# Kernel optimization log

Measured on AMD Instinct MI355X. Metric: run time of the kernel, lower is better.

The kernel has to match this reference:

```python
import jax, jax.numpy as jnp
import numpy as np

B, N, D, H = 4, 2048, 1024, 16
HD = D // H


def setup_inputs() -> dict:
    key = jax.random.key(0)
    ks = jax.random.split(key, 9)
    s = 1.0 / np.sqrt(D)
    return {
        "x": jax.random.normal(ks[0], (B, N, D), jnp.float32),
        "Wq": jax.random.normal(ks[1], (D, D), jnp.float32) * s,
        "bq": jnp.zeros((D,), jnp.float32),
        "Wk": jax.random.normal(ks[2], (D, D), jnp.float32) * s,
        "bk": jnp.zeros((D,), jnp.float32),
        "Wv": jax.random.normal(ks[3], (D, D), jnp.float32) * s,
        "bv": jnp.zeros((D,), jnp.float32),
        "Wo": jax.random.normal(ks[4], (D, D), jnp.float32) * s,
        "bo": jnp.zeros((D,), jnp.float32),
    }


def reference(x, Wq, bq, Wk, bk, Wv, bv, Wo, bo):
    Bx, Nx, Dx = x.shape
    q = x @ Wq + bq  # [B,N,D]
    k = x @ Wk + bk
    v = x @ Wv + bv
    # split heads -> [B,H,N,hd]
    q = q.reshape(Bx, Nx, H, HD).transpose(0, 2, 1, 3)
    k = k.reshape(Bx, Nx, H, HD).transpose(0, 2, 1, 3)
    v = v.reshape(Bx, Nx, H, HD).transpose(0, 2, 1, 3)
    q = q / jnp.sqrt(jnp.asarray(HD, q.dtype))
    scores = jnp.einsum("bhqd,bhkd->bhqk", q, k)
    # causal mask: additive -1e9 strictly above diagonal (matches torch.triu diag=1)
    mask = jnp.triu(jnp.full((Nx, Nx), -1e9, dtype=scores.dtype), k=1)
    probs = jax.nn.softmax(scores + mask, axis=-1)
    out = jnp.einsum("bhqk,bhkd->bhqd", probs, v)  # [B,H,N,hd]
    out = out.transpose(0, 2, 1, 3).reshape(Bx, Nx, Dx)  # concat heads
    return out @ Wo + bo
```

## Files before the change

### kernel.cpp

```cpp
#include <hip/hip_runtime.h>
#include <hip/hip_bf16.h>


#define BB 4
#define NN 2048
#define DD 1024
#define HH 16
#define HD 64
#define MM (BB * NN)

typedef __bf16 bf16;
typedef __bf16 bf16x4 __attribute__((ext_vector_type(4)));
typedef __bf16 bf16x8 __attribute__((ext_vector_type(8)));
typedef float f32x4 __attribute__((ext_vector_type(4)));

__device__ __forceinline__ void async_copy16(bf16* lds, const bf16* g) {
    __builtin_amdgcn_global_load_lds(
        (const __attribute__((address_space(1))) void*)g,
        (__attribute__((address_space(3))) void*)lds, 16, 0, 0);
}

__global__ void prep(const float* __restrict__ x,
                     const float* __restrict__ W0, const float* __restrict__ W1,
                     const float* __restrict__ W2, const float* __restrict__ W3,
                     bf16* __restrict__ xb, bf16* __restrict__ Wt) {
    __shared__ float tile[32][33];
    if (blockIdx.z == 0) {
        int i = (blockIdx.x * 256 + threadIdx.x) * 8;
        float4 a = *(const float4*)&x[i];
        float4 b = *(const float4*)&x[i + 4];
        bf16x8 o;
        o[0] = (bf16)a.x; o[1] = (bf16)a.y; o[2] = (bf16)a.z; o[3] = (bf16)a.w;
        o[4] = (bf16)b.x; o[5] = (bf16)b.y; o[6] = (bf16)b.z; o[7] = (bf16)b.w;
        *(bf16x8*)&xb[i] = o;
    } else {
        int wz = blockIdx.x >> 10;
        int by = (blockIdx.x >> 5) & 31;
        int bx = blockIdx.x & 31;
        const float* W = (wz == 0) ? W0 : (wz == 1) ? W1 : (wz == 2) ? W2 : W3;
        bf16* out = Wt + (size_t)wz * DD * DD;
        int tx = threadIdx.x & 31, ty = threadIdx.x >> 5;
        int x0 = bx * 32, y0 = by * 32;
#pragma unroll
        for (int i = 0; i < 32; i += 8)
            tile[ty + i][tx] = W[(size_t)(y0 + ty + i) * DD + x0 + tx];
        __syncthreads();
#pragma unroll
        for (int i = 0; i < 32; i += 8)
            out[(size_t)(x0 + ty + i) * DD + y0 + tx] = (bf16)tile[tx][ty + i];
    }
}

__global__ __launch_bounds__(512, 4) void gemm_qkv(
    const bf16* __restrict__ A, const bf16* __restrict__ Wt,
    const float* __restrict__ b0, const float* __restrict__ b1,
    const float* __restrict__ b2, bf16* __restrict__ out0,
    bf16* __restrict__ out1, bf16* __restrict__ out2) {
    const int K = DD;
    __shared__ __align__(16) bf16 smem[128 * 136];
    bf16* As = smem;
    bf16* Bs = smem + 256 * 32;
    bf16* Cs = smem;

    int m0 = blockIdx.x * 256;
    int n0 = blockIdx.y * 128;
    int z = blockIdx.z;
    const bf16* Wz = Wt + (size_t)z * DD * DD;
    const float* bias = (z == 0) ? b0 : ((z == 1) ? b1 : b2);
    bf16* out = (z == 0) ? out0 : ((z == 1) ? out1 : out2);
    float scale = (z == 0) ? 0.125f * 1.44269504f : 1.0f;

    int tid = threadIdx.x;
    int w = tid >> 6, lane = tid & 63;
    int wm = w >> 1, wn = w & 1;
    int quad = lane >> 4, l16 = lane & 15;

    f32x4 acc[4][4];
#pragma unroll
    for (int i = 0; i < 4; i++)
#pragma unroll
        for (int j = 0; j < 4; j++) acc[i][j] = (f32x4){0.f, 0.f, 0.f, 0.f};

    for (int k0 = 0; k0 < K; k0 += 32) {
        __syncthreads();
#pragma unroll
        for (int j = 0; j < 2; j++) {
            int c = j * 512 + tid;
            int row = c >> 2, kk = (c & 3) * 8;
            async_copy16(&As[c * 8], &A[(size_t)(m0 + row) * K + k0 + kk]);
        }
        {
            int row = tid >> 2, kk = (tid & 3) * 8;
            async_copy16(&Bs[tid * 8], &Wz[(size_t)(n0 + row) * K + k0 + kk]);
        }
        __syncthreads();

        bf16x8 af[4], bfm[4];
#pragma unroll
        for (int i = 0; i < 4; i++) {
            af[i] = *(const bf16x8*)&As[(wm * 64 + i * 16 + l16) * 32 + quad * 8];
            bfm[i] = *(const bf16x8*)&Bs[(wn * 64 + i * 16 + l16) * 32 + quad * 8];
        }
#pragma unroll
        for (int i = 0; i < 4; i++)
#pragma unroll
            for (int j = 0; j < 4; j++)
                acc[i][j] = __builtin_amdgcn_mfma_f32_16x16x32_bf16(
                    af[i], bfm[j], acc[i][j], 0, 0, 0);
    }

    int bidx = m0 >> 11;
    int tok0 = m0 & (NN - 1);
    int hh0 = n0 >> 6;
    __syncthreads();

#pragma unroll
    for (int pp = 0; pp < 2; pp++) {
        if (pp) __syncthreads();
        if ((wm >> 1) == pp) {
#pragma unroll
            for (int j = 0; j < 4; j++) {
                int nl = wn * 64 + j * 16 + l16;
                float bv = bias[n0 + nl];
#pragma unroll
                for (int i = 0; i < 4; i++) {
#pragma unroll
                    for (int r = 0; r < 4; r++) {
                        int mloc = (wm & 1) * 64 + i * 16 + quad * 4 + r;
                        bf16 v = (bf16)((acc[i][j][r] + bv) * scale);
                        if (z == 2) Cs[nl * 136 + mloc] = v;
                        else        Cs[mloc * 136 + nl] = v;
                    }
                }
            }
        }
        __syncthreads();

        if (z != 2) {
#pragma unroll
            for (int hf = 0; hf < 2; hf++) {
                bf16* base = out +
                    ((size_t)(bidx * HH + hh0 + hf) * NN + tok0 + pp * 128) * HD;
#pragma unroll
                for (int k = 0; k < 2; k++) {
                    int f = k * 4096 + tid * 8;
                    *(bf16x8*)&base[f] =
                        *(const bf16x8*)&Cs[(f >> 6) * 136 + hf * 64 + (f & 63)];
                }
            }
        } else {
#pragma unroll
            for (int k = 0; k < 4; k++) {
                int idx = k * 4096 + tid * 8;
                int nl = idx >> 7;
                int p0 = idx & 127;
                int hf = nl >> 6, hd = nl & 63;
                int base32 = p0 & ~31;
                int qq = (p0 & 31) >> 3;
                const bf16* crow = &Cs[nl * 136];
                bf16x4 lo = *(const bf16x4*)&crow[base32 + qq * 4];
                bf16x4 hi = *(const bf16x4*)&crow[base32 + qq * 4 + 16];
                bf16x8 v = __builtin_shufflevector(lo, hi, 0, 1, 2, 3, 4, 5, 6, 7);
                bf16* dst = out +
                    ((size_t)(bidx * HH + hh0 + hf) * HD + hd) * NN +
                    tok0 + pp * 128 + p0;
                *(bf16x8*)dst = v;
            }
        }
    }
}

__global__ __launch_bounds__(256) void gemm_out(
    const bf16* __restrict__ A, const bf16* __restrict__ Wt,
    const float* __restrict__ bias, float* __restrict__ out) {
    const int K = DD;
    __shared__ __align__(16) bf16 smem[128 * 64];
    bf16* As = smem;
    bf16* Bs = smem + 128 * 32;

    int m0 = blockIdx.x * 128;
    int n0 = blockIdx.y * 128;

    int tid = threadIdx.x;
    int w = tid >> 6, lane = tid & 63;
    int wm = w >> 1, wn = w & 1;
    int quad = lane >> 4, l16 = lane & 15;

    f32x4 acc[4][4];
#pragma unroll
    for (int i = 0; i < 4; i++)
#pragma unroll
        for (int j = 0; j < 4; j++) acc[i][j] = (f32x4){0.f, 0.f, 0.f, 0.f};

    for (int k0 = 0; k0 < K; k0 += 32) {
        __syncthreads();
#pragma unroll
        for (int j = 0; j < 2; j++) {
            int c = j * 256 + w * 64 + lane;
            int row = c >> 2, kk = (c & 3) * 8;
            async_copy16(&As[c * 8], &A[(size_t)(m0 + row) * K + k0 + kk]);
            async_copy16(&Bs[c * 8], &Wt[(size_t)(n0 + row) * K + k0 + kk]);
        }
        __syncthreads();

        bf16x8 af[4], bfm[4];
#pragma unroll
        for (int i = 0; i < 4; i++) {
            af[i] = *(const bf16x8*)&As[(wm * 64 + i * 16 + l16) * 32 + quad * 8];
            bfm[i] = *(const bf16x8*)&Bs[(wn * 64 + i * 16 + l16) * 32 + quad * 8];
        }
#pragma unroll
        for (int i = 0; i < 4; i++)
#pragma unroll
            for (int j = 0; j < 4; j++)
                acc[i][j] = __builtin_amdgcn_mfma_f32_16x16x32_bf16(
                    af[i], bfm[j], acc[i][j], 0, 0, 0);
    }

#pragma unroll
    for (int j = 0; j < 4; j++) {
        int n = n0 + wn * 64 + j * 16 + l16;
        float bv = bias[n];
#pragma unroll
        for (int i = 0; i < 4; i++) {
            int mrow = m0 + wm * 64 + i * 16 + quad * 4;
#pragma unroll
            for (int r = 0; r < 4; r++)
                out[(size_t)(mrow + r) * DD + n] = acc[i][j][r] + bv;
        }
    }
}

__global__ __launch_bounds__(256, 4) void flash_attn(
    const bf16* __restrict__ Q, const bf16* __restrict__ Kg,
    const bf16* __restrict__ Vt_g, bf16* __restrict__ Oc) {
    __shared__ __align__(16) bf16 Ks[2][64 * 72];
    __shared__ __align__(16) bf16 Vs[2][64 * 72];

    int bh = blockIdx.x;
    int b = bh >> 4, h = bh & 15;
    int tid = threadIdx.x;
    int w = tid >> 6, lane = tid & 63;
    int quad = lane >> 4, l16 = lane & 15;

    const bf16* Qb = Q + (size_t)bh * NN * HD;
    const bf16* Kb = Kg + (size_t)bh * NN * HD;
    const bf16* Vtb = Vt_g + (size_t)bh * HD * NN;

    bf16x8 ones8;
#pragma unroll
    for (int i = 0; i < 8; i++) ones8[i] = (bf16)1.0f;

    int kr[2], kc[2];
#pragma unroll
    for (int j = 0; j < 2; j++) {
        int c = j * 256 + tid;
        kr[j] = c >> 3; kc[j] = (c & 7) * 8;
    }

    for (int phase = 0; phase < 2; phase++) {
        int qj = (phase == 0) ? blockIdx.y : (31 - blockIdx.y);
        int q0 = qj * 64;
        int qrow = q0 + w * 16 + l16;

        bf16x8 qf[2];
#pragma unroll
        for (int ks = 0; ks < 2; ks++)
            qf[ks] = *(const bf16x8*)&Qb[(size_t)qrow * HD + ks * 32 + quad * 8];

        f32x4 l_sum = (f32x4){0.f, 0.f, 0.f, 0.f};
        f32x4 o_acc[4];
#pragma unroll
        for (int di = 0; di < 4; di++) o_acc[di] = (f32x4){0.f, 0.f, 0.f, 0.f};

        bf16x8 kreg[2], vreg[2];
#pragma unroll
        for (int j = 0; j < 2; j++) {
            kreg[j] = *(const bf16x8*)&Kb[(size_t)kr[j] * HD + kc[j]];
            vreg[j] = *(const bf16x8*)&Vtb[(size_t)kr[j] * NN + kc[j]];
        }
#pragma unroll
        for (int j = 0; j < 2; j++) {
            *(bf16x8*)&Ks[0][kr[j] * 72 + kc[j]] = kreg[j];
            *(bf16x8*)&Vs[0][kr[j] * 72 + kc[j]] = vreg[j];
        }
        __syncthreads();

        for (int t = 0; t <= qj; t++) {
            int cur = t & 1;
            if (t < qj) {
                int kvn = (t + 1) * 64;
#pragma unroll
                for (int j = 0; j < 2; j++) {
                    kreg[j] = *(const bf16x8*)&Kb[(size_t)(kvn + kr[j]) * HD + kc[j]];
                    vreg[j] = *(const bf16x8*)&Vtb[(size_t)kr[j] * NN + kvn + kc[j]];
                }
            }

            const bf16* Kcur = Ks[cur];
            const bf16* Vcur = Vs[cur];
            int kv0 = t * 64;
            bool diag = (t == qj);
#pragma unroll
            for (int mi = 0; mi < 2; mi++) {
                int ba = 2 * mi, bb = 2 * mi + 1;
                bf16x8 ka0 = *(const bf16x8*)&Kcur[(ba * 16 + l16) * 72 + quad * 8];
                bf16x8 ka1 = *(const bf16x8*)&Kcur[(ba * 16 + l16) * 72 + 32 + quad * 8];
                bf16x8 kb0 = *(const bf16x8*)&Kcur[(bb * 16 + l16) * 72 + quad * 8];
                bf16x8 kb1 = *(const bf16x8*)&Kcur[(bb * 16 + l16) * 72 + 32 + quad * 8];
                f32x4 sa = (f32x4){0.f, 0.f, 0.f, 0.f};
                f32x4 sb = (f32x4){0.f, 0.f, 0.f, 0.f};
                sa = __builtin_amdgcn_mfma_f32_16x16x32_bf16(ka0, qf[0], sa, 0, 0, 0);
                sa = __builtin_amdgcn_mfma_f32_16x16x32_bf16(ka1, qf[1], sa, 0, 0, 0);
                sb = __builtin_amdgcn_mfma_f32_16x16x32_bf16(kb0, qf[0], sb, 0, 0, 0);
                sb = __builtin_amdgcn_mfma_f32_16x16x32_bf16(kb1, qf[1], sb, 0, 0, 0);
                bf16x4 pa4, pb4;
                if (diag) {
                    int kva = kv0 + ba * 16 + quad * 4;
                    int kvb = kv0 + bb * 16 + quad * 4;
#pragma unroll
                    for (int r = 0; r < 4; r++) {
                        pa4[r] = (bf16)((kva + r > qrow) ? 0.f : exp2f(sa[r]));
                        pb4[r] = (bf16)((kvb + r > qrow) ? 0.f : exp2f(sb[r]));
                    }
                } else {
#pragma unroll
                    for (int r = 0; r < 4; r++) {
                        pa4[r] = (bf16)exp2f(sa[r]);
                        pb4[r] = (bf16)exp2f(sb[r]);
                    }
                }
                bf16x8 pfrag = __builtin_shufflevector(pa4, pb4, 0, 1, 2, 3, 4, 5, 6, 7);
                l_sum = __builtin_amdgcn_mfma_f32_16x16x32_bf16(pfrag, ones8, l_sum, 0, 0, 0);
#pragma unroll
                for (int di = 0; di < 4; di++) {
                    bf16x8 vfrag = *(const bf16x8*)&Vcur[(di * 16 + l16) * 72 + mi * 32 + quad * 8];
                    o_acc[di] = __builtin_amdgcn_mfma_f32_16x16x32_bf16(pfrag, vfrag, o_acc[di], 0, 0, 0);
                }
            }

            if (t < qj) {
                bf16* Kn = Ks[cur ^ 1];
                bf16* Vn = Vs[cur ^ 1];
#pragma unroll
                for (int j = 0; j < 2; j++) {
                    *(bf16x8*)&Kn[kr[j] * 72 + kc[j]] = kreg[j];
                    *(bf16x8*)&Vn[kr[j] * 72 + kc[j]] = vreg[j];
                }
            }
            __syncthreads();
        }

#pragma unroll
        for (int r = 0; r < 4; r++) {
            float inv = 1.0f / l_sum[r];
            int tok = q0 + w * 16 + quad * 4 + r;
#pragma unroll
            for (int di = 0; di < 4; di++) {
                int d = h * 64 + di * 16 + l16;
                Oc[((size_t)(b * NN + tok)) * DD + d] = (bf16)(o_acc[di][r] * inv);
            }
        }
    }
}

extern "C" void kernel_launch(void* const* d_in, const int* in_sizes, int n_in,
                              void* d_out, int out_size, void* d_ws, size_t ws_size,
                              hipStream_t stream) {
    const float* x  = (const float*)d_in[0];
    const float* Wq = (const float*)d_in[1];
    const float* bq = (const float*)d_in[2];
    const float* Wk = (const float*)d_in[3];
    const float* bk = (const float*)d_in[4];
    const float* Wv = (const float*)d_in[5];
    const float* bv = (const float*)d_in[6];
    const float* Wo = (const float*)d_in[7];
    const float* bo = (const float*)d_in[8];

    const size_t need = (size_t)(8388608ull * 5 + 4194304ull) * sizeof(bf16);
    if (ws_size < need) return;

    bf16* ws = (bf16*)d_ws;
    bf16* xb = ws;
    bf16* wt = xb + (size_t)MM * DD;
    bf16* Qw = wt + 4ull * DD * DD;
    bf16* Kw = Qw + (size_t)MM * DD;
    bf16* Vw = Kw + (size_t)MM * DD;
    bf16* Aw = Vw + (size_t)MM * DD;

    prep<<<dim3(4096, 1, 2), 256, 0, stream>>>(x, Wq, Wk, Wv, Wo, xb, wt);

    gemm_qkv<<<dim3(MM / 256, DD / 128, 3), 512, 0, stream>>>(
        xb, wt, bq, bk, bv, Qw, Kw, Vw);

    flash_attn<<<dim3(BB * HH, 16), 256, 0, stream>>>(Qw, Kw, Vw, Aw);

    gemm_out<<<dim3(MM / 128, DD / 128), 256, 0, stream>>>(
        Aw, wt + 3ull * DD * DD, bo, (float*)d_out);
}
```

Baseline: 265.0 us.

## Fuse Q/K/V projections into one block sharing the loaded A tile

The QKV GEMM no longer launches one grid slice per projection. Each 256-thread block now loads a 128-row tile of x once and multiplies it against all three weight tiles, holding three accumulator sets. This cuts global and LDS traffic for the activation matrix. In exchange the block keeps 192 accumulator floats per thread, has fewer threads and blocks (launch bounds 256,1), and runs three serialized epilogues, so occupancy and register pressure may suffer.

```diff
diff --git a/kernel.cpp b/kernel.cpp
--- a/kernel.cpp
+++ b/kernel.cpp
@@ -51,7 +51,7 @@
     }
 }
 
-__global__ __launch_bounds__(512, 4) void gemm_qkv(
+__global__ __launch_bounds__(256, 1) void gemm_qkv(
     const bf16* __restrict__ A, const bf16* __restrict__ Wt,
     const float* __restrict__ b0, const float* __restrict__ b1,
     const float* __restrict__ b2, bf16* __restrict__ out0,
@@ -59,54 +59,57 @@
     const int K = DD;
     __shared__ __align__(16) bf16 smem[128 * 136];
     bf16* As = smem;
-    bf16* Bs = smem + 256 * 32;
+    bf16* Bs = smem + 4096;
     bf16* Cs = smem;
 
-    int m0 = blockIdx.x * 256;
+    int m0 = blockIdx.x * 128;
     int n0 = blockIdx.y * 128;
-    int z = blockIdx.z;
-    const bf16* Wz = Wt + (size_t)z * DD * DD;
-    const float* bias = (z == 0) ? b0 : ((z == 1) ? b1 : b2);
-    bf16* out = (z == 0) ? out0 : ((z == 1) ? out1 : out2);
-    float scale = (z == 0) ? 0.125f * 1.44269504f : 1.0f;
 
     int tid = threadIdx.x;
     int w = tid >> 6, lane = tid & 63;
     int wm = w >> 1, wn = w & 1;
     int quad = lane >> 4, l16 = lane & 15;
 
-    f32x4 acc[4][4];
-#pragma unroll
-    for (int i = 0; i < 4; i++)
-#pragma unroll
-        for (int j = 0; j < 4; j++) acc[i][j] = (f32x4){0.f, 0.f, 0.f, 0.f};
+    f32x4 acc[3][4][4];
+#pragma unroll
+    for (int zz = 0; zz < 3; zz++)
+#pragma unroll
+        for (int i = 0; i < 4; i++)
+#pragma unroll
+            for (int j = 0; j < 4; j++)
+                acc[zz][i][j] = (f32x4){0.f, 0.f, 0.f, 0.f};
 
     for (int k0 = 0; k0 < K; k0 += 32) {
         __syncthreads();
 #pragma unroll
         for (int j = 0; j < 2; j++) {
-            int c = j * 512 + tid;
+            int c = j * 256 + w * 64 + lane;
             int row = c >> 2, kk = (c & 3) * 8;
             async_copy16(&As[c * 8], &A[(size_t)(m0 + row) * K + k0 + kk]);
-        }
-        {
-            int row = tid >> 2, kk = (tid & 3) * 8;
-            async_copy16(&Bs[tid * 8], &Wz[(size_t)(n0 + row) * K + k0 + kk]);
-        }
-        __syncthreads();
-
-        bf16x8 af[4], bfm[4];
-#pragma unroll
-        for (int i = 0; i < 4; i++) {
+#pragma unroll
+            for (int zz = 0; zz < 3; zz++)
+                async_copy16(&Bs[zz * 4096 + c * 8],
+                             &Wt[(size_t)zz * DD * DD + (size_t)(n0 + row) * K + k0 + kk]);
+        }
+        __syncthreads();
+
+        bf16x8 af[4];
+#pragma unroll
+        for (int i = 0; i < 4; i++)
             af[i] = *(const bf16x8*)&As[(wm * 64 + i * 16 + l16) * 32 + quad * 8];
-            bfm[i] = *(const bf16x8*)&Bs[(wn * 64 + i * 16 + l16) * 32 + quad * 8];
-        }
-#pragma unroll
-        for (int i = 0; i < 4; i++)
-#pragma unroll
-            for (int j = 0; j < 4; j++)
-                acc[i][j] = __builtin_amdgcn_mfma_f32_16x16x32_bf16(
-                    af[i], bfm[j], acc[i][j], 0, 0, 0);
+#pragma unroll
+        for (int zz = 0; zz < 3; zz++) {
+            bf16x8 bfm[4];
+#pragma unroll
+            for (int i = 0; i < 4; i++)
+                bfm[i] = *(const bf16x8*)&Bs[zz * 4096 + (wn * 64 + i * 16 + l16) * 32 + quad * 8];
+#pragma unroll
+            for (int i = 0; i < 4; i++)
+#pragma unroll
+                for (int j = 0; j < 4; j++)
+                    acc[zz][i][j] = __builtin_amdgcn_mfma_f32_16x16x32_bf16(
+                        af[i], bfm[j], acc[zz][i][j], 0, 0, 0);
+        }
     }
 
     int bidx = m0 >> 11;
@@ -115,56 +118,57 @@
     __syncthreads();
 
 #pragma unroll
-    for (int pp = 0; pp < 2; pp++) {
-        if (pp) __syncthreads();
-        if ((wm >> 1) == pp) {
-#pragma unroll
-            for (int j = 0; j < 4; j++) {
-                int nl = wn * 64 + j * 16 + l16;
-                float bv = bias[n0 + nl];
-#pragma unroll
-                for (int i = 0; i < 4; i++) {
-#pragma unroll
-                    for (int r = 0; r < 4; r++) {
-                        int mloc = (wm & 1) * 64 + i * 16 + quad * 4 + r;
-                        bf16 v = (bf16)((acc[i][j][r] + bv) * scale);
-                        if (z == 2) Cs[nl * 136 + mloc] = v;
-                        else        Cs[mloc * 136 + nl] = v;
-                    }
-                }
-            }
-        }
-        __syncthreads();
-
-        if (z != 2) {
+    for (int zz = 0; zz < 3; zz++) {
+        if (zz) __syncthreads();
+        const float* bias = (zz == 0) ? b0 : ((zz == 1) ? b1 : b2);
+        bf16* out = (zz == 0) ? out0 : ((zz == 1) ? out1 : out2);
+        float scale = (zz == 0) ? 0.125f * 1.44269504f : 1.0f;
+
+#pragma unroll
+        for (int j = 0; j < 4; j++) {
+            int nl = wn * 64 + j * 16 + l16;
+            float bv = bias[n0 + nl];
+#pragma unroll
+            for (int i = 0; i < 4; i++) {
+#pragma unroll
+                for (int r = 0; r < 4; r++) {
+                    int ml = wm * 64 + i * 16 + quad * 4 + r;
+                    bf16 v = (bf16)((acc[zz][i][j][r] + bv) * scale);
+                    if (zz == 2) Cs[nl * 136 + ml] = v;
+                    else         Cs[ml * 136 + nl] = v;
+                }
+            }
+        }
+        __syncthreads();
+
+        if (zz != 2) {
 #pragma unroll
             for (int hf = 0; hf < 2; hf++) {
-                bf16* base = out +
-                    ((size_t)(bidx * HH + hh0 + hf) * NN + tok0 + pp * 128) * HD;
-#pragma unroll
-                for (int k = 0; k < 2; k++) {
-                    int f = k * 4096 + tid * 8;
-                    *(bf16x8*)&base[f] =
-                        *(const bf16x8*)&Cs[(f >> 6) * 136 + hf * 64 + (f & 63)];
+                bf16* base = out + ((size_t)(bidx * HH + hh0 + hf) * NN + tok0) * HD;
+#pragma unroll
+                for (int k = 0; k < 4; k++) {
+                    int f = k * 2048 + tid * 8;
+                    int tok = f >> 6, hd = f & 63;
+                    *(bf16x8*)&base[f] = *(const bf16x8*)&Cs[tok * 136 + hf * 64 + hd];
                 }
             }
         } else {
 #pragma unroll
-            for (int k = 0; k < 4; k++) {
-                int idx = k * 4096 + tid * 8;
-                int nl = idx >> 7;
-                int p0 = idx & 127;
-                int hf = nl >> 6, hd = nl & 63;
-                int base32 = p0 & ~31;
-                int qq = (p0 & 31) >> 3;
-                const bf16* crow = &Cs[nl * 136];
-                bf16x4 lo = *(const bf16x4*)&crow[base32 + qq * 4];
-                bf16x4 hi = *(const bf16x4*)&crow[base32 + qq * 4 + 16];
-                bf16x8 v = __builtin_shufflevector(lo, hi, 0, 1, 2, 3, 4, 5, 6, 7);
-                bf16* dst = out +
-                    ((size_t)(bidx * HH + hh0 + hf) * HD + hd) * NN +
-                    tok0 + pp * 128 + p0;
-                *(bf16x8*)dst = v;
+            for (int hf = 0; hf < 2; hf++) {
+#pragma unroll
+                for (int k = 0; k < 4; k++) {
+                    int hd = k * 16 + (tid >> 4);
+                    int p0 = (tid & 15) * 8;
+                    int base32 = p0 & ~31;
+                    int qq = (p0 & 31) >> 3;
+                    const bf16* crow = &Cs[(hf * 64 + hd) * 136];
+                    bf16x4 lo = *(const bf16x4*)&crow[base32 + qq * 4];
+                    bf16x4 hi = *(const bf16x4*)&crow[base32 + qq * 4 + 16];
+                    bf16x8 v = __builtin_shufflevector(lo, hi, 0, 1, 2, 3, 4, 5, 6, 7);
+                    bf16* dst = out +
+                        ((size_t)(bidx * HH + hh0 + hf) * HD + hd) * NN + tok0 + p0;
+                    *(bf16x8*)dst = v;
+                }
             }
         }
     }
@@ -390,7 +394,7 @@
 
     prep<<<dim3(4096, 1, 2), 256, 0, stream>>>(x, Wq, Wk, Wv, Wo, xb, wt);
 
-    gemm_qkv<<<dim3(MM / 256, DD / 128, 3), 512, 0, stream>>>(
+    gemm_qkv<<<dim3(MM / 128, DD / 128), 256, 0, stream>>>(
         xb, wt, bq, bk, bv, Qw, Kw, Vw);
 
     flash_attn<<<dim3(BB * HH, 16), 256, 0, stream>>>(Qw, Kw, Vw, Aw);
```

After: 280.5 us. 5.9% more time.
